# Optimization experiments

Hardware: AMD Instinct MI355X
Metric: run time of the kernel (lower is better)

Reference implementation:

```python
import jax, jax.numpy as jnp
import numpy as np

B, S, D = 1, 2048, 2048
H, KVH, HD = 16, 8, 128
ROPE_THETA = 1e6
P_POW, C_SHIFT = 8, 7.0
MASK_VAL = -7.0  # = -c so masked bpmax base ~ scores only (finite under ^8)


def rotate_half(x):
    x1, x2 = jnp.split(x, 2, axis=-1)
    return jnp.concatenate([-x2, x1], axis=-1)


def setup_inputs() -> dict:
    key = jax.random.key(0)
    ks = jax.random.split(key, 10)
    hidden_states = jax.random.normal(ks[0], (B, S, D), dtype=jnp.float32)
    # RoPE tables (Qwen3-style, theta=1e6)
    inv_freq = 1.0 / (ROPE_THETA ** (jnp.arange(0, HD, 2, dtype=jnp.float32) / HD))
    freqs = jnp.arange(S, dtype=jnp.float32)[:, None] * inv_freq[None, :]
    emb = jnp.concatenate([freqs, freqs], axis=-1)  # [S, HD]
    cos = jnp.broadcast_to(jnp.cos(emb)[None], (B, S, HD)).astype(jnp.float32)
    sin = jnp.broadcast_to(jnp.sin(emb)[None], (B, S, HD)).astype(jnp.float32)
    sc = D ** -0.5
    q_proj_w = jax.random.normal(ks[1], (D, H * HD), dtype=jnp.float32) * sc
    k_proj_w = jax.random.normal(ks[2], (D, KVH * HD), dtype=jnp.float32) * sc
    v_proj_w = jax.random.normal(ks[3], (D, KVH * HD), dtype=jnp.float32) * sc
    o_proj_w = jax.random.normal(ks[4], (H * HD, D), dtype=jnp.float32) * (H * HD) ** -0.5
    q_norm_w = jnp.ones((HD,), dtype=jnp.float32)
    k_norm_w = jnp.ones((HD,), dtype=jnp.float32)
    # Stored RMSNorm denominators (rsqrt-like buffers from training), ~O(1)
    q_denom = 0.5 + jax.random.uniform(ks[5], (B, S, H, 1), dtype=jnp.float32)
    k_denom = 0.5 + jax.random.uniform(ks[6], (B, S, KVH, 1), dtype=jnp.float32)
    # Stored bpmax normalizer buffer rd (per-head, per-query-row)
    rd = 5.0 + 10.0 * jax.random.uniform(ks[7], (1, H, S, 1), dtype=jnp.float32)
    # Causal mask with MASK_VAL for masked positions (finite under bpmax)
    causal = jnp.tril(jnp.ones((S, S), dtype=bool))
    attention_mask = jnp.where(causal, 0.0, MASK_VAL)[None, None].astype(jnp.float32)
    return {
        'hidden_states': hidden_states, 'cos': cos, 'sin': sin,
        'q_proj_w': q_proj_w, 'k_proj_w': k_proj_w, 'v_proj_w': v_proj_w,
        'o_proj_w': o_proj_w, 'q_norm_w': q_norm_w, 'k_norm_w': k_norm_w,
        'q_denom': q_denom, 'k_denom': k_denom, 'rd': rd,
        'attention_mask': attention_mask,
    }


def reference(hidden_states, cos, sin, q_proj_w, k_proj_w, v_proj_w, o_proj_w,
              q_norm_w, k_norm_w, q_denom, k_denom, rd, attention_mask):
    b, s, d = hidden_states.shape
    hd = q_norm_w.shape[0]
    scaling = hd ** -0.5
    # Projections + per-head RMSNorm (eval path: stored denominator buffer)
    q = (hidden_states @ q_proj_w).reshape(b, s, -1, hd)
    q = (q_norm_w * (q * q_denom[:, :s])).transpose(0, 2, 1, 3)   # [B,H,S,hd]
    k = (hidden_states @ k_proj_w).reshape(b, s, -1, hd)
    k = (k_norm_w * (k * k_denom[:, :s])).transpose(0, 2, 1, 3)   # [B,KVH,S,hd]
    v = (hidden_states @ v_proj_w).reshape(b, s, -1, hd).transpose(0, 2, 1, 3)
    # RoPE
    cos_ = cos[:, None, :, :]
    sin_ = sin[:, None, :, :]
    q = q * cos_ + rotate_half(q) * sin_
    k = k * cos_ + rotate_half(k) * sin_
    # GQA: repeat kv heads
    groups = q.shape[1] // k.shape[1]
    k = jnp.repeat(k, groups, axis=1)
    v = jnp.repeat(v, groups, axis=1)
    # Scores + mask + bpmax power-law normalization (eval path)
    aw = jnp.einsum('bhqd,bhkd->bhqk', q, k) * scaling
    aw = aw + attention_mask[:, :, :, :s]
    aw = ((aw + C_SHIFT) / rd[:, :, :s, :]) ** P_POW
    # Attention output + output projection
    out = jnp.einsum('bhqk,bhkd->bhqd', aw, v)
    out = out.transpose(0, 2, 1, 3).reshape(b, s, -1)
    return out @ o_proj_w
```

## Files before the change

### kernel.cpp

```cpp
#include <hip/hip_runtime.h>
#include <cstdint>
#include <cstddef>


namespace {
constexpr int kS = 2048;
constexpr int kD = 2048;
constexpr int kH = 16;
constexpr int kKVH = 8;
constexpr int kHD = 128;
constexpr float kScale = 0.08838834764831845f;
constexpr size_t MB = 1u << 20;
}

using f32x4 = __attribute__((ext_vector_type(4))) float;
using bfrag = __attribute__((ext_vector_type(8))) short;
using float4v = __attribute__((ext_vector_type(4))) float;
using short4v = __attribute__((ext_vector_type(4))) short;

__device__ __forceinline__ unsigned short f2b(float f) {
  union { float f; unsigned u; } x; x.f = f;
  unsigned r = x.u + 0x7FFFu + ((x.u >> 16) & 1u);
  return (unsigned short)(r >> 16);
}

__device__ __forceinline__ float b2f(unsigned short u) {
  union { unsigned u; float f; } x; x.u = ((unsigned)u) << 16;
  return x.f;
}

__device__ __forceinline__ void gload_lds16(const void* g, void* l) {
  __builtin_amdgcn_global_load_lds(
      (const __attribute__((address_space(1))) unsigned*)g,
      (__attribute__((address_space(3))) unsigned*)l, 16, 0, 0);
}

__global__ __launch_bounds__(256) void qwen_cast_bf16(const float* __restrict__ in,
                                                      unsigned short* __restrict__ out,
                                                      int n4) {
  int i = blockIdx.x * 256 + threadIdx.x;
  if (i >= n4) return;
  float4v v = *(const float4v*)(in + (size_t)i * 4);
  short4v o;
  o[0] = (short)f2b(v[0]); o[1] = (short)f2b(v[1]);
  o[2] = (short)f2b(v[2]); o[3] = (short)f2b(v[3]);
  int i4 = i * 4;
  int row = i4 >> 11, col = i4 & 2047;
  int scol = col ^ ((row & 3) << 3);
  *(short4v*)(out + ((size_t)row << 11) + scol) = o;
}

__global__ __launch_bounds__(256) void qwen_tw(const float* __restrict__ in, int R, int C,
                                               unsigned short* __restrict__ out, int ldo) {
  __shared__ float t[64][65];
  int c0 = blockIdx.x * 64, r0 = blockIdx.y * 64;
  int tr = threadIdx.x >> 6, tc = threadIdx.x & 63;
#pragma unroll
  for (int p = 0; p < 16; ++p) {
    int i = p * 4 + tr;
    t[i][tc] = in[(size_t)(r0 + i) * C + c0 + tc];
  }
  __syncthreads();
#pragma unroll
  for (int p = 0; p < 16; ++p) {
    int i = p * 4 + tr;
    int orow = c0 + i;
    int ocol = r0 + tc;
    int scol = ocol ^ ((orow & 3) << 3);
    out[(size_t)orow * ldo + scol] = f2b(t[tc][i]);
  }
}

template <int BM, bool BF16OUT>
__global__ __launch_bounds__(256) void qwen_gemm_bt(const unsigned short* __restrict__ A,
                                                    const unsigned short* __restrict__ Bt,
                                                    void* __restrict__ Cv,
                                                    int M, int N, int K) {
  __shared__ unsigned short As[2][BM * 32];
  __shared__ unsigned short Bs[2][128 * 32];
  constexpr int MR = BM / 32;
  const int nwg = gridDim.x * gridDim.y;
  int lin = blockIdx.y * gridDim.x + blockIdx.x;
  if ((nwg & 7) == 0) { int qq = nwg >> 3; lin = (lin & 7) * qq + (lin >> 3); }
  const int bxx = lin % gridDim.x, byy = lin / gridDim.x;
  const int tid = threadIdx.x, lane = tid & 63, w = tid >> 6;
  const int wr = w >> 1, wc = w & 1;
  const int row0 = bxx * BM, col0 = byy * 128;
  f32x4 acc[MR][4] = {};
  const int koff = (lane >> 4) << 3;
  const int swz = (lane & 3) << 3;
  const int kread = koff ^ swz;
  const int rA = wr * (BM / 2) + (lane & 15);
  const int rB = wc * 64 + (lane & 15);

  auto stage = [&](int kt, int b) {
#pragma unroll
    for (int c = 0; c < BM / 64; ++c) {
      int off = (c * 256 + tid) * 16;
      int e = off >> 1;
      int r = e >> 5, cc = e & 31;
      gload_lds16(A + (size_t)(row0 + r) * K + kt + cc, (char*)(&As[b][0]) + off);
    }
#pragma unroll
    for (int c = 0; c < 2; ++c) {
      int off = (c * 256 + tid) * 16;
      int e = off >> 1;
      int r = e >> 5, cc = e & 31;
      gload_lds16(Bt + (size_t)(col0 + r) * K + kt + cc, (char*)(&Bs[b][0]) + off);
    }
  };

  const int nk = K >> 5;
  stage(0, 0);
  asm volatile("s_waitcnt vmcnt(0)" ::: "memory");
  __builtin_amdgcn_s_barrier();
  int buf = 0;
#pragma unroll 1
  for (int t = 0; t < nk; ++t) {
    if (t + 1 < nk) stage((t + 1) << 5, buf ^ 1);
    bfrag aF[MR], bF[4];
#pragma unroll
    for (int m = 0; m < MR; ++m)
      aF[m] = *(const bfrag*)(&As[buf][0] + (rA + m * 16) * 32 + kread);
#pragma unroll
    for (int n = 0; n < 4; ++n)
      bF[n] = *(const bfrag*)(&Bs[buf][0] + (rB + n * 16) * 32 + kread);
#pragma unroll
    for (int m = 0; m < MR; ++m)
#pragma unroll
      for (int n = 0; n < 4; ++n)
        acc[m][n] = __builtin_amdgcn_mfma_f32_16x16x32_bf16(aF[m], bF[n], acc[m][n], 0, 0, 0);
    asm volatile("s_waitcnt vmcnt(0)" ::: "memory");
    __builtin_amdgcn_s_barrier();
    buf ^= 1;
  }
  const int cr = (lane >> 4) << 2;
  const int cc2 = lane & 15;
#pragma unroll
  for (int m = 0; m < MR; ++m)
#pragma unroll
    for (int n = 0; n < 4; ++n) {
      int r = row0 + wr * (BM / 2) + m * 16 + cr;
      int c = col0 + wc * 64 + n * 16 + cc2;
#pragma unroll
      for (int j = 0; j < 4; ++j) {
        if constexpr (BF16OUT) {
          ((unsigned short*)Cv)[(size_t)(r + j) * N + c] = f2b(acc[m][n][j]);
        } else {
          ((float*)Cv)[(size_t)(r + j) * N + c] = acc[m][n][j];
        }
      }
    }
}

__global__ __launch_bounds__(256) void qwen_rope(const unsigned short* __restrict__ Cq16,
                                                 const float* __restrict__ cosb,
                                                 const float* __restrict__ sinb,
                                                 const float* __restrict__ qnw,
                                                 const float* __restrict__ knw,
                                                 const float* __restrict__ qden,
                                                 const float* __restrict__ kden,
                                                 unsigned short* __restrict__ Qb,
                                                 unsigned short* __restrict__ Kswz) {
  __shared__ unsigned short SMrow[4096];
  const int s = blockIdx.x;
  const int t = threadIdx.x;
  {
    const char* src = (const char*)(Cq16 + (size_t)s * 4096);
    gload_lds16(src + t * 16, (char*)SMrow + t * 16);
    gload_lds16(src + 4096 + t * 16, (char*)SMrow + 4096 + t * 16);
  }
  __syncthreads();
  const float* cs = cosb + (size_t)s * kHD;
  const float* sn = sinb + (size_t)s * kHD;
#pragma unroll
  for (int rep = 0; rep < 8; ++rep) {
    int idx = rep * 256 + t;
    int h = idx >> 7, d = idx & 127;
    float dn = qden[s * kH + h];
    float v = b2f(SMrow[idx]) * dn * qnw[d];
    float pv = b2f(SMrow[(h << 7) + (d ^ 64)]) * dn * qnw[d ^ 64];
    float rot = (d < 64) ? -pv : pv;
    Qb[((size_t)h * kS + s) * kHD + d] = f2b(v * cs[d] + rot * sn[d]);
  }
  const int kt = s >> 6, key = s & 63;
#pragma unroll
  for (int rep = 0; rep < 4; ++rep) {
    int idx = rep * 256 + t;
    int h = idx >> 7, d = idx & 127;
    float dn = kden[s * kKVH + h];
    float v = b2f(SMrow[2048 + idx]) * dn * knw[d];
    float pv = b2f(SMrow[2048 + (h << 7) + (d ^ 64)]) * dn * knw[d ^ 64];
    float rot = (d < 64) ? -pv : pv;
    size_t rowi = ((size_t)(h * 32 + kt) * 64 + key) * 128;
    Kswz[rowi + (d ^ ((key & 7) << 3))] = f2b(v * cs[d] + rot * sn[d]);
  }
}

__global__ __launch_bounds__(256) void qwen_vtr(const unsigned short* __restrict__ Cq16,
                                                unsigned short* __restrict__ Vswz) {
  __shared__ unsigned short t[64][66];
  int kvh = blockIdx.x, st = blockIdx.y, dt = blockIdx.z;
  int s0 = st * 64, d0 = dt * 64;
  int tr = threadIdx.x >> 6, tc = threadIdx.x & 63;
#pragma unroll
  for (int p = 0; p < 16; ++p) {
    int i = p * 4 + tr;
    t[i][tc] = Cq16[(size_t)(s0 + i) * 4096 + 3072 + (kvh << 7) + d0 + tc];
  }
  __syncthreads();
#pragma unroll
  for (int p = 0; p < 16; ++p) {
    int i = p * 4 + tr;
    int d = d0 + i;
    size_t rowi = ((size_t)(kvh * 32 + st) * 128 + d) * 64;
    Vswz[rowi + (tc ^ ((d & 15) << 2))] = t[tc][i];
  }
}

#define STAGE8(cc, bb)                                                 \
  do {                                                                 \
    const char* ks_ = Ksrc + ((size_t)(cc) << 14) + tid * 16;          \
    const char* vs_ = Vsrc + ((size_t)(cc) << 14) + tid * 16;          \
    char* kd_ = (char*)(&KV[bb][0]) + tid * 16;                        \
    char* vd_ = (char*)(&KV[2 + (bb)][0]) + tid * 16;                  \
    _Pragma("unroll") for (int it = 0; it < 4; ++it) {                 \
      gload_lds16(ks_ + it * 4096, kd_ + it * 4096);                   \
      gload_lds16(vs_ + it * 4096, vd_ + it * 4096);                   \
    }                                                                  \
  } while (0)

__global__ __launch_bounds__(256, 2) void qwen_attn(const unsigned short* __restrict__ Qb,
                                                    const unsigned short* __restrict__ Kswz,
                                                    const unsigned short* __restrict__ Vswz,
                                                    const float* __restrict__ rd,
                                                    float* __restrict__ Pacc) {
  __shared__ unsigned short KV[4][8192];
  const int bid = blockIdx.x;
  const int kvh = bid & 7;
  const int x = bid >> 3;
  const int half = x >> 5;
  const int x5 = x & 31;
  const int hb = x5 >> 4;
  const int t0 = x5 & 15;
  const int qt = half ? t0 : (15 - t0);
  const int parity = half;
  const int h = kvh * 2 + hb;
  const int q0 = qt * 128;
  const int nlc = qt + 1;
  const int tid = threadIdx.x, lane = tid & 63, w = tid >> 6;
  const int l15 = lane & 15, g = lane >> 4;
  const int qw0 = q0 + w * 32;
  const int qlim0 = qw0 + l15;
  const int qlim1 = qw0 + 16 + l15;
  const int swzK = (l15 & 7) << 3;
  const int swzV = l15 << 2;

  bfrag qF[2][4];
#pragma unroll
  for (int qs = 0; qs < 2; ++qs)
#pragma unroll
    for (int dc = 0; dc < 4; ++dc)
      qF[qs][dc] = *(const bfrag*)(Qb + ((size_t)h * kS + qw0 + qs * 16 + l15) * kHD +
                                   dc * 32 + g * 8);
  const float inv[2] = {1.0f / rd[(size_t)h * kS + qlim0],
                        1.0f / rd[(size_t)h * kS + qlim1]};

  const char* Ksrc = (const char*)Kswz + ((size_t)(kvh * 32) << 14);
  const char* Vsrc = (const char*)Vswz + ((size_t)(kvh * 32) << 14);

  f32x4 outa[2][8] = {};

  STAGE8(parity, 0);
#pragma unroll 1
  for (int lc = 0; lc < nlc; ++lc) {
    const int c = parity + 2 * lc;
    const int b = lc & 1;
    asm volatile("s_waitcnt vmcnt(0)" ::: "memory");
    __builtin_amdgcn_s_barrier();
    if (lc + 1 < nlc) STAGE8(c + 2, b ^ 1);
    __builtin_amdgcn_s_setprio(1);
    const unsigned short* Kbuf = &KV[b][0];
    const unsigned short* Vbuf = &KV[2 + b][0];
    f32x4 sc[2][4] = {};
#pragma unroll
    for (int t4 = 0; t4 < 4; ++t4) {
      const unsigned short* kr = Kbuf + (t4 * 16 + l15) * 128;
#pragma unroll
      for (int dc = 0; dc < 4; ++dc) {
        bfrag kf = *(const bfrag*)(kr + ((dc * 32 + g * 8) ^ swzK));
        sc[0][t4] = __builtin_amdgcn_mfma_f32_16x16x32_bf16(kf, qF[0][dc], sc[0][t4], 0, 0, 0);
        sc[1][t4] = __builtin_amdgcn_mfma_f32_16x16x32_bf16(kf, qF[1][dc], sc[1][t4], 0, 0, 0);
      }
    }
    const int kbase = c * 64;
    const bool full = (kbase + 63 <= qw0);
    union { bfrag f; unsigned u[4]; } pb[2][2];
#pragma unroll
    for (int qs = 0; qs < 2; ++qs) {
      const int ql = qs ? qlim1 : qlim0;
      const float iv = inv[qs];
#pragma unroll
      for (int t4 = 0; t4 < 4; ++t4) {
        unsigned short bb[4];
#pragma unroll
        for (int rr = 0; rr < 4; ++rr) {
          float tt = sc[qs][t4][rr] * kScale;
          int key = kbase + t4 * 16 + g * 4 + rr;
          tt += (full || key <= ql) ? 7.0f : 0.0f;
          float y = tt * iv;
          float y2 = y * y, y4 = y2 * y2;
          bb[rr] = f2b(y4 * y4);
        }
        pb[qs][t4 >> 1].u[(t4 & 1) * 2 + 0] = (unsigned)bb[0] | ((unsigned)bb[1] << 16);
        pb[qs][t4 >> 1].u[(t4 & 1) * 2 + 1] = (unsigned)bb[2] | ((unsigned)bb[3] << 16);
      }
    }
#pragma unroll
    for (int dt = 0; dt < 8; ++dt) {
      const unsigned short* vr = Vbuf + (dt * 16 + l15) * 64;
#pragma unroll
      for (int pr = 0; pr < 2; ++pr) {
        union { bfrag f; short4v h4[2]; } va;
        va.h4[0] = *(const short4v*)(vr + ((pr * 32 + g * 4) ^ swzV));
        va.h4[1] = *(const short4v*)(vr + ((pr * 32 + 16 + g * 4) ^ swzV));
        outa[0][dt] = __builtin_amdgcn_mfma_f32_16x16x32_bf16(va.f, pb[0][pr].f, outa[0][dt], 0, 0, 0);
        outa[1][dt] = __builtin_amdgcn_mfma_f32_16x16x32_bf16(va.f, pb[1][pr].f, outa[1][dt], 0, 0, 0);
      }
    }
    __builtin_amdgcn_s_setprio(0);
  }
  {
    float* Po = Pacc + (((size_t)(h * 16 + qt) * 2 + parity) << 14);
#pragma unroll
    for (int qs = 0; qs < 2; ++qs) {
      const int qrow = w * 32 + qs * 16 + l15;
#pragma unroll
      for (int dt = 0; dt < 8; ++dt) {
        f32x4 v = outa[qs][dt];
        *(f32x4*)(Po + qrow * 128 + dt * 16 + g * 4) = v;
      }
    }
  }
}

__global__ __launch_bounds__(256) void qwen_ared(const float* __restrict__ Pacc,
                                                 unsigned short* __restrict__ AO) {
  const int unit = blockIdx.x;
  const int h = unit >> 4, qt = unit & 15;
  const float* P0 = Pacc + ((size_t)unit << 15);
  const float* P1 = P0 + 16384;
  const int t = threadIdx.x;
#pragma unroll
  for (int i = 0; i < 16; ++i) {
    int idx = (i * 256 + t) * 4;
    f32x4 a = *(const f32x4*)(P0 + idx);
    f32x4 b = *(const f32x4*)(P1 + idx);
    int qrow = idx >> 7, d = idx & 127;
    int q = qt * 128 + qrow;
    int col = h * 128 + d;
    short4v o;
    o[0] = (short)f2b(a[0] + b[0]); o[1] = (short)f2b(a[1] + b[1]);
    o[2] = (short)f2b(a[2] + b[2]); o[3] = (short)f2b(a[3] + b[3]);
    *(short4v*)(AO + (size_t)q * kD + (col ^ ((q & 3) << 3))) = o;
  }
}

extern "C" void kernel_launch(void* const* d_in, const int* in_sizes, int n_in,
                              void* d_out, int out_size, void* d_ws, size_t ws_size,
                              hipStream_t stream) {
  (void)in_sizes; (void)n_in; (void)out_size; (void)ws_size;
  const float* hidden = (const float*)d_in[0];
  const float* cosb   = (const float*)d_in[1];
  const float* sinb   = (const float*)d_in[2];
  const float* qw     = (const float*)d_in[3];
  const float* kw     = (const float*)d_in[4];
  const float* vw     = (const float*)d_in[5];
  const float* ow     = (const float*)d_in[6];
  const float* qnw    = (const float*)d_in[7];
  const float* knw    = (const float*)d_in[8];
  const float* qden   = (const float*)d_in[9];
  const float* kden   = (const float*)d_in[10];
  const float* rd     = (const float*)d_in[11];
  float* out = (float*)d_out;

  char* ws = (char*)d_ws;
  unsigned short* hsb  = (unsigned short*)(ws + 0 * MB);
  unsigned short* Wt   = (unsigned short*)(ws + 8 * MB);
  unsigned short* Cq16 = (unsigned short*)(ws + 24 * MB);
  float*          Pacc = (float*)(ws + 24 * MB);
  unsigned short* Qb   = (unsigned short*)(ws + 56 * MB);
  unsigned short* Kswz = (unsigned short*)(ws + 64 * MB);
  unsigned short* Vswz = (unsigned short*)(ws + 68 * MB);
  unsigned short* AO   = (unsigned short*)(ws + 72 * MB);
  unsigned short* Ot   = (unsigned short*)(ws + 80 * MB);

  qwen_cast_bf16<<<4096, 256, 0, stream>>>(hidden, hsb, 2048 * 2048 / 4);
  qwen_tw<<<dim3(32, 32), 256, 0, stream>>>(qw, 2048, 2048, Wt, 2048);
  qwen_tw<<<dim3(16, 32), 256, 0, stream>>>(kw, 2048, 1024, Wt + (size_t)2048 * 2048, 2048);
  qwen_tw<<<dim3(16, 32), 256, 0, stream>>>(vw, 2048, 1024, Wt + (size_t)3072 * 2048, 2048);
  qwen_tw<<<dim3(32, 32), 256, 0, stream>>>(ow, 2048, 2048, Ot, 2048);
  qwen_gemm_bt<128, true><<<dim3(16, 32), 256, 0, stream>>>(hsb, Wt, Cq16, 2048, 4096, 2048);
  qwen_rope<<<2048, 256, 0, stream>>>(Cq16, cosb, sinb, qnw, knw, qden, kden, Qb, Kswz);
  qwen_vtr<<<dim3(8, 32, 2), 256, 0, stream>>>(Cq16, Vswz);
  qwen_attn<<<512, 256, 0, stream>>>(Qb, Kswz, Vswz, rd, Pacc);
  qwen_ared<<<256, 256, 0, stream>>>(Pacc, AO);
  qwen_gemm_bt<64, false><<<dim3(32, 16), 256, 0, stream>>>(AO, Ot, out, 2048, 2048, 2048);
}
```

Baseline: 165.1 us.

## Use 256x128 GEMM tiles with triple-buffered loads and split-K output projection

Measured after the change: 202.5 us. +22.7%, slower.

```diff
diff --git a/kernel.cpp b/kernel.cpp
--- a/kernel.cpp
+++ b/kernel.cpp
@@ -71,86 +71,96 @@
   }
 }
 
-template <int BM, bool BF16OUT>
-__global__ __launch_bounds__(256) void qwen_gemm_bt(const unsigned short* __restrict__ A,
-                                                    const unsigned short* __restrict__ Bt,
-                                                    void* __restrict__ Cv,
-                                                    int M, int N, int K) {
-  __shared__ unsigned short As[2][BM * 32];
-  __shared__ unsigned short Bs[2][128 * 32];
-  constexpr int MR = BM / 32;
+template <int OUTMODE>
+__global__ __launch_bounds__(256, 1) void qwen_gemm_big(const unsigned short* __restrict__ A,
+                                                        const unsigned short* __restrict__ Bt,
+                                                        void* __restrict__ Cv,
+                                                        int M, int N, int Kfull, int KS) {
+  __shared__ unsigned short As[3][256 * 32];
+  __shared__ unsigned short Bs[3][128 * 32];
   const int nwg = gridDim.x * gridDim.y;
   int lin = blockIdx.y * gridDim.x + blockIdx.x;
-  if ((nwg & 7) == 0) { int qq = nwg >> 3; lin = (lin & 7) * qq + (lin >> 3); }
+  { int qq = nwg >> 3; lin = (lin & 7) * qq + (lin >> 3); }
   const int bxx = lin % gridDim.x, byy = lin / gridDim.x;
+  const int k0 = blockIdx.z * KS;
   const int tid = threadIdx.x, lane = tid & 63, w = tid >> 6;
   const int wr = w >> 1, wc = w & 1;
-  const int row0 = bxx * BM, col0 = byy * 128;
-  f32x4 acc[MR][4] = {};
+  const int row0 = bxx * 256, col0 = byy * 128;
+  f32x4 acc[8][4] = {};
   const int koff = (lane >> 4) << 3;
-  const int swz = (lane & 3) << 3;
-  const int kread = koff ^ swz;
-  const int rA = wr * (BM / 2) + (lane & 15);
+  const int kread = koff ^ ((lane & 3) << 3);
+  const int rA = wr * 128 + (lane & 15);
   const int rB = wc * 64 + (lane & 15);
 
   auto stage = [&](int kt, int b) {
 #pragma unroll
-    for (int c = 0; c < BM / 64; ++c) {
+    for (int c = 0; c < 4; ++c) {
       int off = (c * 256 + tid) * 16;
       int e = off >> 1;
       int r = e >> 5, cc = e & 31;
-      gload_lds16(A + (size_t)(row0 + r) * K + kt + cc, (char*)(&As[b][0]) + off);
+      gload_lds16(A + (size_t)(row0 + r) * Kfull + k0 + kt + cc, (char*)(&As[b][0]) + off);
     }
 #pragma unroll
     for (int c = 0; c < 2; ++c) {
       int off = (c * 256 + tid) * 16;
       int e = off >> 1;
       int r = e >> 5, cc = e & 31;
-      gload_lds16(Bt + (size_t)(col0 + r) * K + kt + cc, (char*)(&Bs[b][0]) + off);
+      gload_lds16(Bt + (size_t)(col0 + r) * Kfull + k0 + kt + cc, (char*)(&Bs[b][0]) + off);
     }
   };
 
-  const int nk = K >> 5;
+  const int nk = KS >> 5;
   stage(0, 0);
-  asm volatile("s_waitcnt vmcnt(0)" ::: "memory");
-  __builtin_amdgcn_s_barrier();
-  int buf = 0;
+  stage(32, 1);
 #pragma unroll 1
   for (int t = 0; t < nk; ++t) {
-    if (t + 1 < nk) stage((t + 1) << 5, buf ^ 1);
-    bfrag aF[MR], bF[4];
-#pragma unroll
-    for (int m = 0; m < MR; ++m)
+    if (t + 1 < nk) {
+      asm volatile("s_waitcnt vmcnt(6)" ::: "memory");
+    } else {
+      asm volatile("s_waitcnt vmcnt(0)" ::: "memory");
+    }
+    __builtin_amdgcn_s_barrier();
+    if (t + 2 < nk) stage((t + 2) << 5, (t + 2) % 3);
+    const int buf = t % 3;
+    bfrag aF[8], bF[4];
+#pragma unroll
+    for (int m = 0; m < 8; ++m)
       aF[m] = *(const bfrag*)(&As[buf][0] + (rA + m * 16) * 32 + kread);
 #pragma unroll
     for (int n = 0; n < 4; ++n)
       bF[n] = *(const bfrag*)(&Bs[buf][0] + (rB + n * 16) * 32 + kread);
 #pragma unroll
-    for (int m = 0; m < MR; ++m)
+    for (int m = 0; m < 8; ++m)
 #pragma unroll
       for (int n = 0; n < 4; ++n)
         acc[m][n] = __builtin_amdgcn_mfma_f32_16x16x32_bf16(aF[m], bF[n], acc[m][n], 0, 0, 0);
-    asm volatile("s_waitcnt vmcnt(0)" ::: "memory");
-    __builtin_amdgcn_s_barrier();
-    buf ^= 1;
   }
   const int cr = (lane >> 4) << 2;
   const int cc2 = lane & 15;
 #pragma unroll
-  for (int m = 0; m < MR; ++m)
+  for (int m = 0; m < 8; ++m)
 #pragma unroll
     for (int n = 0; n < 4; ++n) {
-      int r = row0 + wr * (BM / 2) + m * 16 + cr;
+      int r = row0 + wr * 128 + m * 16 + cr;
       int c = col0 + wc * 64 + n * 16 + cc2;
 #pragma unroll
       for (int j = 0; j < 4; ++j) {
-        if constexpr (BF16OUT) {
+        if constexpr (OUTMODE == 0) {
           ((unsigned short*)Cv)[(size_t)(r + j) * N + c] = f2b(acc[m][n][j]);
         } else {
-          ((float*)Cv)[(size_t)(r + j) * N + c] = acc[m][n][j];
+          ((float*)Cv)[(size_t)blockIdx.z * M * N + (size_t)(r + j) * N + c] = acc[m][n][j];
         }
       }
     }
+}
+
+__global__ __launch_bounds__(256) void qwen_ored(const float* __restrict__ P,
+                                                 float* __restrict__ out) {
+  int i = (blockIdx.x * 256 + threadIdx.x) * 4;
+  f32x4 a = *(const f32x4*)(P + i);
+  f32x4 b = *(const f32x4*)(P + (size_t)2048 * 2048 + i);
+  f32x4 s = a + b;
+  *(f32x4*)(out + i) = s;
 }
 
 __global__ __launch_bounds__(256) void qwen_rope(const unsigned short* __restrict__ Cq16,
@@ -389,6 +399,7 @@
   unsigned short* Wt   = (unsigned short*)(ws + 8 * MB);
   unsigned short* Cq16 = (unsigned short*)(ws + 24 * MB);
   float*          Pacc = (float*)(ws + 24 * MB);
+  float*          Pocc = (float*)(ws + 24 * MB);
   unsigned short* Qb   = (unsigned short*)(ws + 56 * MB);
   unsigned short* Kswz = (unsigned short*)(ws + 64 * MB);
   unsigned short* Vswz = (unsigned short*)(ws + 68 * MB);
@@ -400,10 +411,11 @@
   qwen_tw<<<dim3(16, 32), 256, 0, stream>>>(kw, 2048, 1024, Wt + (size_t)2048 * 2048, 2048);
   qwen_tw<<<dim3(16, 32), 256, 0, stream>>>(vw, 2048, 1024, Wt + (size_t)3072 * 2048, 2048);
   qwen_tw<<<dim3(32, 32), 256, 0, stream>>>(ow, 2048, 2048, Ot, 2048);
-  qwen_gemm_bt<128, true><<<dim3(16, 32), 256, 0, stream>>>(hsb, Wt, Cq16, 2048, 4096, 2048);
+  qwen_gemm_big<0><<<dim3(8, 32, 1), 256, 0, stream>>>(hsb, Wt, Cq16, 2048, 4096, 2048, 2048);
   qwen_rope<<<2048, 256, 0, stream>>>(Cq16, cosb, sinb, qnw, knw, qden, kden, Qb, Kswz);
   qwen_vtr<<<dim3(8, 32, 2), 256, 0, stream>>>(Cq16, Vswz);
   qwen_attn<<<512, 256, 0, stream>>>(Qb, Kswz, Vswz, rd, Pacc);
   qwen_ared<<<256, 256, 0, stream>>>(Pacc, AO);
-  qwen_gemm_bt<64, false><<<dim3(32, 16), 256, 0, stream>>>(AO, Ot, out, 2048, 2048, 2048);
-}
+  qwen_gemm_big<1><<<dim3(8, 16, 2), 256, 0, stream>>>(AO, Ot, Pocc, 2048, 2048, 2048, 1024);
+  qwen_ored<<<4096, 256, 0, stream>>>(Pocc, out);
+}
```
